# Kernel optimization log

Hardware: AMD Instinct MI355X
Metric: run time of the kernel (lower is better)

Reference implementation:

```python
import jax, jax.numpy as jnp
import numpy as np

EPS = 1e-6
NUM_HEADS = 16


def _layer_norm(x, alpha, beta):
    # Custom LN: unbiased std, divides by (std + eps) -- matches source exactly.
    mean = jnp.mean(x, axis=-1, keepdims=True)
    std = jnp.std(x, axis=-1, keepdims=True, ddof=1)
    return alpha * (x - mean) / (std + EPS) + beta


def _mha(x, wq, bq, wk, bk, wv, bv, wo, bo):
    B, S, D = x.shape
    H = NUM_HEADS
    Dh = D // H
    q = (x @ wq.T + bq).reshape(B, S, H, Dh)
    k = (x @ wk.T + bk).reshape(B, S, H, Dh)
    v = (x @ wv.T + bv).reshape(B, S, H, Dh)
    scores = jnp.einsum('bqhd,bkhd->bhqk', q, k) / jnp.sqrt(jnp.float32(Dh)).astype(x.dtype)
    p = jax.nn.softmax(scores, axis=-1)
    out = jnp.einsum('bhqk,bkhd->bqhd', p, v).reshape(B, S, D)
    return out @ wo.T + bo


def _ffn(x, w1, b1, w2, b2):
    return jax.nn.relu(x @ w1.T + b1) @ w2.T + b2


def setup_inputs() -> dict:
    key = jax.random.key(0)
    ks = jax.random.split(key, 8)
    B, S, D, Hf = 8, 1024, 1024, 4096
    s = lambda d: 1.0 / np.sqrt(d)
    return {
        'x': jax.random.normal(ks[0], (B, S, D), jnp.float32),
        'src_mask': jnp.ones((B, 1, 1, S), jnp.int32),
        'wq': jax.random.normal(ks[1], (D, D), jnp.float32) * s(D),
        'bq': jnp.zeros((D,), jnp.float32),
        'wk': jax.random.normal(ks[2], (D, D), jnp.float32) * s(D),
        'bk': jnp.zeros((D,), jnp.float32),
        'wv': jax.random.normal(ks[3], (D, D), jnp.float32) * s(D),
        'bv': jnp.zeros((D,), jnp.float32),
        'wo': jax.random.normal(ks[4], (D, D), jnp.float32) * s(D),
        'bo': jnp.zeros((D,), jnp.float32),
        'w1': jax.random.normal(ks[5], (Hf, D), jnp.float32) * s(D),
        'b1': jnp.zeros((Hf,), jnp.float32),
        'w2': jax.random.normal(ks[6], (D, Hf), jnp.float32) * s(Hf),
        'b2': jnp.zeros((D,), jnp.float32),
        'alpha': jnp.ones((D,), jnp.float32),
        'beta': jnp.zeros((D,), jnp.float32),
    }


def reference(x, src_mask, wq, bq, wk, bk, wv, bv, wo, bo, w1, b1, w2, b2, alpha, beta):
    # src_mask is unused in the source's attention implementation (faithful).
    # Pre-LN residual block 1: attention (shared LN params alpha/beta).
    x = x + _mha(_layer_norm(x, alpha, beta), wq, bq, wk, bk, wv, bv, wo, bo)
    # Pre-LN residual block 2: feed-forward (same shared LN instance).
    x = x + _ffn(_layer_norm(x, alpha, beta), w1, b1, w2, b2)
    return x
```

## Files before the change

kernel.cpp:

```cpp
#include <hip/hip_runtime.h>
#include <hip/hip_bf16.h>
#include <stdint.h>

typedef __bf16 bf16;
typedef __attribute__((ext_vector_type(8))) __bf16 bf16x8;
typedef __attribute__((ext_vector_type(4))) __bf16 bf16x4;
typedef __attribute__((ext_vector_type(4))) float floatx4;

typedef __attribute__((address_space(3))) uint32_t* lds_u32p;
typedef const __attribute__((address_space(1))) uint32_t* glb_u32p;

__device__ __forceinline__ void gload16(void* lds, const void* g) {
  __builtin_amdgcn_global_load_lds((glb_u32p)(uintptr_t)g,
                                   (lds_u32p)(uintptr_t)lds, 16, 0, 0);
}

__global__ __launch_bounds__(256) void detect_kernel(
    const unsigned short* __restrict__ xr, int* __restrict__ flag) {
  __shared__ int cnt;
  if (threadIdx.x == 0) cnt = 0;
  __syncthreads();
  int c = 0;
  for (int i = threadIdx.x; i < 8192; i += 256) {
    unsigned short e = (xr[i] >> 7) & 0xFF;
    if (e >= 0x90) ++c;
  }
  atomicAdd(&cnt, c);
  __syncthreads();
  if (threadIdx.x == 0) *flag = (cnt > 64) ? 1 : 0;
}

#define NCONV 14
struct ConvArgs {
  const void* src[NCONV];
  bf16* dst[NCONV];
  int nelem[NCONV];
  int bstart[NCONV + 1];
};

__global__ __launch_bounds__(256) void convert_kernel(ConvArgs a, const int* __restrict__ flag) {
  const int isf = *flag;
  const int bx = blockIdx.x;
  int t = 0;
  #pragma unroll
  for (int i = 1; i < NCONV; ++i)
    if (bx >= a.bstart[i]) t = i;
  const int base = (bx - a.bstart[t]) * 2048 + threadIdx.x * 8;
  if (base >= a.nelem[t]) return;
  if (isf) {
    const float* s = (const float*)a.src[t] + base;
    const float4 x0 = *reinterpret_cast<const float4*>(s);
    const float4 x1 = *reinterpret_cast<const float4*>(s + 4);
    bf16x8 o;
    o[0] = (bf16)x0.x; o[1] = (bf16)x0.y; o[2] = (bf16)x0.z; o[3] = (bf16)x0.w;
    o[4] = (bf16)x1.x; o[5] = (bf16)x1.y; o[6] = (bf16)x1.z; o[7] = (bf16)x1.w;
    *reinterpret_cast<bf16x8*>(a.dst[t] + base) = o;
  } else {
    *reinterpret_cast<bf16x8*>(a.dst[t] + base) =
        *reinterpret_cast<const bf16x8*>((const bf16*)a.src[t] + base);
  }
}

__global__ __launch_bounds__(256) void ln_kernel(
    const void* __restrict__ x, const bf16* __restrict__ alpha,
    const bf16* __restrict__ beta, bf16* __restrict__ y,
    const int* __restrict__ flag, int x_ext) {
  const int isf = *flag;
  const int row = blockIdx.x;
  const int tid = threadIdx.x;

  float v0, v1, v2, v3;
  if (x_ext && isf) {
    const float4 xv = *reinterpret_cast<const float4*>(
        (const float*)x + (size_t)row * 1024 + tid * 4);
    v0 = xv.x; v1 = xv.y; v2 = xv.z; v3 = xv.w;
  } else {
    const bf16x4 xv = *reinterpret_cast<const bf16x4*>(
        (const bf16*)x + (size_t)row * 1024 + tid * 4);
    v0 = (float)xv[0]; v1 = (float)xv[1]; v2 = (float)xv[2]; v3 = (float)xv[3];
  }
  float s = v0 + v1 + v2 + v3;
  float ss = v0 * v0 + v1 * v1 + v2 * v2 + v3 * v3;
  #pragma unroll
  for (int off = 32; off > 0; off >>= 1) {
    s += __shfl_down(s, off);
    ss += __shfl_down(ss, off);
  }
  __shared__ float red[8];
  __shared__ float s_mean, s_inv;
  const int w = tid >> 6, lane = tid & 63;
  if (lane == 0) { red[w] = s; red[4 + w] = ss; }
  __syncthreads();
  if (tid == 0) {
    float S = red[0] + red[1] + red[2] + red[3];
    float SS = red[4] + red[5] + red[6] + red[7];
    float mean = S * (1.0f / 1024.0f);
    float var = (SS - 1024.0f * mean * mean) * (1.0f / 1023.0f);
    var = fmaxf(var, 0.0f);
    s_mean = mean;
    s_inv = 1.0f / (sqrtf(var) + 1e-6f);
  }
  __syncthreads();
  const float mean = s_mean, inv = s_inv;
  const bf16x4 av = *reinterpret_cast<const bf16x4*>(alpha + tid * 4);
  const bf16x4 bv = *reinterpret_cast<const bf16x4*>(beta + tid * 4);
  bf16x4 out;
  out[0] = (bf16)((float)av[0] * (v0 - mean) * inv + (float)bv[0]);
  out[1] = (bf16)((float)av[1] * (v1 - mean) * inv + (float)bv[1]);
  out[2] = (bf16)((float)av[2] * (v2 - mean) * inv + (float)bv[2]);
  out[3] = (bf16)((float)av[3] * (v3 - mean) * inv + (float)bv[3]);
  *reinterpret_cast<bf16x4*>(y + (size_t)row * 1024 + tid * 4) = out;
}

template <bool RELU, bool RES>
__global__ __launch_bounds__(256) void gemm_bt(
    const bf16* __restrict__ A, const bf16* __restrict__ W,
    const bf16* __restrict__ bias, const void* __restrict__ res,
    void* __restrict__ C, int M, int N, int K,
    const int* __restrict__ flag, int res_ext, int out_ext, int row0) {
  __shared__ bf16 As[128 * 64];
  __shared__ bf16 Bs[128 * 64];
  const int isf = *flag;
  const int tid = threadIdx.x;
  const int m0 = blockIdx.x * 128, n0 = blockIdx.y * 128;
  const int wave = tid >> 6, lane = tid & 63;
  const int wm = (wave >> 1) * 64, wn = (wave & 1) * 64;
  const int lrow = lane & 15, quad = lane >> 4;

  const int srow = lane >> 3;
  const int gchunk = (lane & 7) ^ srow;
  const bf16* Ab = A + (size_t)m0 * K;
  const bf16* Wb = W + (size_t)n0 * K;

  floatx4 acc[4][4] = {};

  for (int k0 = 0; k0 < K; k0 += 64) {
    __syncthreads();
    #pragma unroll
    for (int t = 0; t < 4; ++t) {
      const int r = t * 32 + wave * 8;
      gload16(&As[r * 64], Ab + (size_t)(r + srow) * K + k0 + gchunk * 8);
      gload16(&Bs[r * 64], Wb + (size_t)(r + srow) * K + k0 + gchunk * 8);
    }
    __syncthreads();

    #pragma unroll
    for (int ks = 0; ks < 2; ++ks) {
      const int cswz = ((ks * 4 + quad) ^ (lrow & 7)) * 8;
      bf16x8 af[4], bw[4];
      #pragma unroll
      for (int i = 0; i < 4; ++i) {
        af[i] = *reinterpret_cast<const bf16x8*>(&As[(wm + i * 16 + lrow) * 64 + cswz]);
        bw[i] = *reinterpret_cast<const bf16x8*>(&Bs[(wn + i * 16 + lrow) * 64 + cswz]);
      }
      #pragma unroll
      for (int i = 0; i < 4; ++i)
        #pragma unroll
        for (int j = 0; j < 4; ++j)
          acc[i][j] = __builtin_amdgcn_mfma_f32_16x16x32_bf16(af[i], bw[j], acc[i][j], 0, 0, 0);
    }
  }

  #pragma unroll
  for (int j = 0; j < 4; ++j) {
    const int col = n0 + wn + j * 16 + lrow;
    const float bv = (float)bias[col];
    #pragma unroll
    for (int i = 0; i < 4; ++i) {
      #pragma unroll
      for (int r = 0; r < 4; ++r) {
        const int row = m0 + wm + i * 16 + quad * 4 + r;
        float v = acc[i][j][r] + bv;
        if (RELU) v = fmaxf(v, 0.0f);
        if (RES) {
          const size_t ridx = (size_t)row * N + col;
          v += (res_ext && isf) ? ((const float*)res)[ridx]
                                : (float)((const bf16*)res)[ridx];
        }
        const size_t oidx = (size_t)(row0 + row) * N + col;
        if (out_ext && isf) ((float*)C)[oidx] = v;
        else ((bf16*)C)[oidx] = (bf16)v;
      }
    }
  }
}

template <bool RELU, bool RES>
__global__ __launch_bounds__(256) void gemm_n64(
    const bf16* __restrict__ A, const bf16* __restrict__ W,
    const bf16* __restrict__ bias, const void* __restrict__ res,
    void* __restrict__ C, int M, int N, int K,
    const int* __restrict__ flag, int res_ext, int out_ext, int row0) {
  __shared__ bf16 As[128 * 64];
  __shared__ bf16 Bs[64 * 64];
  const int isf = *flag;
  const int tid = threadIdx.x;
  const int m0 = blockIdx.x * 128, n0 = blockIdx.y * 64;
  const int wave = tid >> 6, lane = tid & 63;
  const int wm = (wave >> 1) * 64, wn = (wave & 1) * 32;
  const int lrow = lane & 15, quad = lane >> 4;

  const int srow = lane >> 3;
  const int gchunk = (lane & 7) ^ srow;
  const bf16* Ab = A + (size_t)m0 * K;
  const bf16* Wb = W + (size_t)n0 * K;

  floatx4 acc[4][2] = {};

  for (int k0 = 0; k0 < K; k0 += 64) {
    __syncthreads();
    #pragma unroll
    for (int t = 0; t < 4; ++t) {
      const int r = t * 32 + wave * 8;
      gload16(&As[r * 64], Ab + (size_t)(r + srow) * K + k0 + gchunk * 8);
    }
    #pragma unroll
    for (int t = 0; t < 2; ++t) {
      const int r = t * 32 + wave * 8;
      gload16(&Bs[r * 64], Wb + (size_t)(r + srow) * K + k0 + gchunk * 8);
    }
    __syncthreads();

    #pragma unroll
    for (int ks = 0; ks < 2; ++ks) {
      const int cswz = ((ks * 4 + quad) ^ (lrow & 7)) * 8;
      bf16x8 af[4], bw[2];
      #pragma unroll
      for (int i = 0; i < 4; ++i)
        af[i] = *reinterpret_cast<const bf16x8*>(&As[(wm + i * 16 + lrow) * 64 + cswz]);
      #pragma unroll
      for (int j = 0; j < 2; ++j)
        bw[j] = *reinterpret_cast<const bf16x8*>(&Bs[(wn + j * 16 + lrow) * 64 + cswz]);
      #pragma unroll
      for (int i = 0; i < 4; ++i)
        #pragma unroll
        for (int j = 0; j < 2; ++j)
          acc[i][j] = __builtin_amdgcn_mfma_f32_16x16x32_bf16(af[i], bw[j], acc[i][j], 0, 0, 0);
    }
  }

  #pragma unroll
  for (int j = 0; j < 2; ++j) {
    const int col = n0 + wn + j * 16 + lrow;
    const float bv = (float)bias[col];
    #pragma unroll
    for (int i = 0; i < 4; ++i) {
      #pragma unroll
      for (int r = 0; r < 4; ++r) {
        const int row = m0 + wm + i * 16 + quad * 4 + r;
        float v = acc[i][j][r] + bv;
        if (RELU) v = fmaxf(v, 0.0f);
        if (RES) {
          const size_t ridx = (size_t)row * N + col;
          v += (res_ext && isf) ? ((const float*)res)[ridx]
                                : (float)((const bf16*)res)[ridx];
        }
        const size_t oidx = (size_t)(row0 + row) * N + col;
        if (out_ext && isf) ((float*)C)[oidx] = v;
        else ((bf16*)C)[oidx] = (bf16)v;
      }
    }
  }
}

__global__ __launch_bounds__(256) void gemm_qkv(
    const bf16* __restrict__ A,
    const bf16* __restrict__ Wq, const bf16* __restrict__ Wk, const bf16* __restrict__ Wv,
    const bf16* __restrict__ Bq, const bf16* __restrict__ Bk, const bf16* __restrict__ Bv,
    bf16* __restrict__ Oq, bf16* __restrict__ Ok, bf16* __restrict__ Ov) {
  const int z = blockIdx.z;
  const bf16* W = (z == 0) ? Wq : (z == 1) ? Wk : Wv;
  const bf16* bias = (z == 0) ? Bq : (z == 1) ? Bk : Bv;
  bf16* C = (z == 0) ? Oq : (z == 1) ? Ok : Ov;
  const int K = 1024, N = 1024;

  __shared__ bf16 As[128 * 64];
  __shared__ bf16 Bs[128 * 64];
  const int tid = threadIdx.x;
  const int m0 = blockIdx.x * 128, n0 = blockIdx.y * 128;
  const int wave = tid >> 6, lane = tid & 63;
  const int wm = (wave >> 1) * 64, wn = (wave & 1) * 64;
  const int lrow = lane & 15, quad = lane >> 4;

  const int srow = lane >> 3;
  const int gchunk = (lane & 7) ^ srow;
  const bf16* Ab = A + (size_t)m0 * K;
  const bf16* Wb = W + (size_t)n0 * K;

  floatx4 acc[4][4] = {};

  for (int k0 = 0; k0 < K; k0 += 64) {
    __syncthreads();
    #pragma unroll
    for (int t = 0; t < 4; ++t) {
      const int r = t * 32 + wave * 8;
      gload16(&As[r * 64], Ab + (size_t)(r + srow) * K + k0 + gchunk * 8);
      gload16(&Bs[r * 64], Wb + (size_t)(r + srow) * K + k0 + gchunk * 8);
    }
    __syncthreads();

    #pragma unroll
    for (int ks = 0; ks < 2; ++ks) {
      const int cswz = ((ks * 4 + quad) ^ (lrow & 7)) * 8;
      bf16x8 af[4], bw[4];
      #pragma unroll
      for (int i = 0; i < 4; ++i) {
        af[i] = *reinterpret_cast<const bf16x8*>(&As[(wm + i * 16 + lrow) * 64 + cswz]);
        bw[i] = *reinterpret_cast<const bf16x8*>(&Bs[(wn + i * 16 + lrow) * 64 + cswz]);
      }
      #pragma unroll
      for (int i = 0; i < 4; ++i)
        #pragma unroll
        for (int j = 0; j < 4; ++j)
          acc[i][j] = __builtin_amdgcn_mfma_f32_16x16x32_bf16(af[i], bw[j], acc[i][j], 0, 0, 0);
    }
  }

  #pragma unroll
  for (int j = 0; j < 4; ++j) {
    const int col = n0 + wn + j * 16 + lrow;
    const float bv = (float)bias[col];
    #pragma unroll
    for (int i = 0; i < 4; ++i) {
      #pragma unroll
      for (int r = 0; r < 4; ++r) {
        const int row = m0 + wm + i * 16 + quad * 4 + r;
        C[(size_t)row * N + col] = (bf16)(acc[i][j][r] + bv);
      }
    }
  }
}

__global__ __launch_bounds__(256) void attn_kernel(
    const bf16* __restrict__ Qg, const bf16* __restrict__ Kg,
    const bf16* __restrict__ Vg, bf16* __restrict__ Og) {
  __shared__ bf16 Ks[64][72];
  __shared__ bf16 Vts[64][72];
  __shared__ bf16 Ps[4][32][72];

  const int tid = threadIdx.x, wave = tid >> 6, lane = tid & 63;
  const int lrow = lane & 15, quad = lane >> 4;
  const int bq = blockIdx.x, h = blockIdx.y, b = blockIdx.z;
  const int q0 = bq * 128 + wave * 32;

  bf16x8 qa[2][2];
  #pragma unroll
  for (int t = 0; t < 2; ++t) {
    const bf16* qbase = Qg + (size_t)(b * 1024 + q0 + t * 16 + lrow) * 1024 + h * 64;
    qa[t][0] = *reinterpret_cast<const bf16x8*>(qbase + quad * 8);
    qa[t][1] = *reinterpret_cast<const bf16x8*>(qbase + 32 + quad * 8);
  }

  const int skp = tid >> 2, sdd = (tid & 3) * 16;
  const int vkp = tid & 63, vdg = wave * 16;

  floatx4 o[2][4] = {};
  float lsum[2][4] = {};

  for (int kc = 0; kc < 1024; kc += 64) {
    __syncthreads();
    {
      const bf16* ksrc = Kg + (size_t)(b * 1024 + kc + skp) * 1024 + h * 64 + sdd;
      *reinterpret_cast<bf16x8*>(&Ks[skp][sdd]) = *reinterpret_cast<const bf16x8*>(ksrc);
      *reinterpret_cast<bf16x8*>(&Ks[skp][sdd + 8]) = *reinterpret_cast<const bf16x8*>(ksrc + 8);

      const bf16* vsrc = Vg + (size_t)(b * 1024 + kc + vkp) * 1024 + h * 64 + vdg;
      bf16x8 v0 = *reinterpret_cast<const bf16x8*>(vsrc);
      bf16x8 v1 = *reinterpret_cast<const bf16x8*>(vsrc + 8);
      #pragma unroll
      for (int j = 0; j < 8; ++j) {
        Vts[vdg + j][vkp] = v0[j];
        Vts[vdg + 8 + j][vkp] = v1[j];
      }
    }
    __syncthreads();

    #pragma unroll
    for (int t = 0; t < 2; ++t) {
      floatx4 s[4] = {};
      #pragma unroll
      for (int kt = 0; kt < 4; ++kt) {
        bf16x8 kb0 = *reinterpret_cast<const bf16x8*>(&Ks[kt * 16 + lrow][quad * 8]);
        bf16x8 kb1 = *reinterpret_cast<const bf16x8*>(&Ks[kt * 16 + lrow][32 + quad * 8]);
        s[kt] = __builtin_amdgcn_mfma_f32_16x16x32_bf16(qa[t][0], kb0, s[kt], 0, 0, 0);
        s[kt] = __builtin_amdgcn_mfma_f32_16x16x32_bf16(qa[t][1], kb1, s[kt], 0, 0, 0);
      }
      #pragma unroll
      for (int r = 0; r < 4; ++r) {
        const float p0 = __expf(s[0][r] * 0.125f);
        const float p1 = __expf(s[1][r] * 0.125f);
        const float p2 = __expf(s[2][r] * 0.125f);
        const float p3 = __expf(s[3][r] * 0.125f);
        lsum[t][r] += (p0 + p1) + (p2 + p3);
        const int qr = t * 16 + quad * 4 + r;
        Ps[wave][qr][lrow] = (bf16)p0;
        Ps[wave][qr][16 + lrow] = (bf16)p1;
        Ps[wave][qr][32 + lrow] = (bf16)p2;
        Ps[wave][qr][48 + lrow] = (bf16)p3;
      }
    }

    __builtin_amdgcn_wave_barrier();

    #pragma unroll
    for (int t = 0; t < 2; ++t) {
      const bf16x8 pf0 = *reinterpret_cast<const bf16x8*>(&Ps[wave][t * 16 + lrow][quad * 8]);
      const bf16x8 pf1 = *reinterpret_cast<const bf16x8*>(&Ps[wave][t * 16 + lrow][32 + quad * 8]);
      #pragma unroll
      for (int j = 0; j < 4; ++j) {
        bf16x8 vb0 = *reinterpret_cast<const bf16x8*>(&Vts[j * 16 + lrow][quad * 8]);
        bf16x8 vb1 = *reinterpret_cast<const bf16x8*>(&Vts[j * 16 + lrow][32 + quad * 8]);
        o[t][j] = __builtin_amdgcn_mfma_f32_16x16x32_bf16(pf0, vb0, o[t][j], 0, 0, 0);
        o[t][j] = __builtin_amdgcn_mfma_f32_16x16x32_bf16(pf1, vb1, o[t][j], 0, 0, 0);
      }
    }
  }

  #pragma unroll
  for (int t = 0; t < 2; ++t) {
    #pragma unroll
    for (int r = 0; r < 4; ++r) {
      float l = lsum[t][r];
      #pragma unroll
      for (int off = 1; off < 16; off <<= 1) l += __shfl_xor(l, off);
      const float inv = 1.0f / l;
      const size_t qrow = (size_t)(b * 1024 + q0 + t * 16 + quad * 4 + r);
      #pragma unroll
      for (int j = 0; j < 4; ++j)
        Og[qrow * 1024 + h * 64 + j * 16 + lrow] = (bf16)(o[t][j][r] * inv);
    }
  }
}

extern "C" void kernel_launch(void* const* d_in, const int* in_sizes, int n_in,
                              void* d_out, int out_size, void* d_ws, size_t ws_size,
                              hipStream_t stream) {
  const void* p[16];
  {
    int j = 0;
    for (int i = 0; i < 16; ++i) {
      if (i == 1) {
        if (j < n_in && in_sizes[j] == 8192) p[i] = d_in[j++];
        else p[i] = nullptr;
        continue;
      }
      p[i] = (j < n_in) ? d_in[j++] : nullptr;
    }
  }
  const void* x = p[0];

  char* ws = (char*)d_ws;
  int* flag = (int*)ws;
  char* wsc = ws + 256;

  const int wsz[NCONV] = {1048576, 1048576, 1048576, 1048576, 4194304, 4194304,
                          1024, 1024, 1024, 1024, 4096, 1024, 1024, 1024};
  const int wsrc[NCONV] = {2, 4, 6, 8, 10, 12, 3, 5, 7, 9, 11, 13, 14, 15};
  ConvArgs ca;
  bf16* cptr[NCONV];
  size_t off = 0;
  int bacc = 0;
  for (int i = 0; i < NCONV; ++i) {
    cptr[i] = (bf16*)(wsc + off);
    off += (size_t)wsz[i] * sizeof(bf16);
    ca.src[i] = p[wsrc[i]];
    ca.dst[i] = cptr[i];
    ca.nelem[i] = wsz[i];
    ca.bstart[i] = bacc;
    bacc += (wsz[i] + 2047) / 2048;
  }
  ca.bstart[NCONV] = bacc;
  const bf16 *wq_c = cptr[0], *wk_c = cptr[1], *wv_c = cptr[2], *wo_c = cptr[3];
  const bf16 *w1_c = cptr[4], *w2_c = cptr[5];
  const bf16 *bq_c = cptr[6], *bk_c = cptr[7], *bv_c = cptr[8], *bo_c = cptr[9];
  const bf16 *b1_c = cptr[10], *b2_c = cptr[11], *al_c = cptr[12], *be_c = cptr[13];

  char* base = wsc + ((off + 255) & ~(size_t)255);
  const size_t SZ = (size_t)8192 * 1024 * sizeof(bf16);
  bf16* s1 = (bf16*)(base);
  bf16* s0 = (bf16*)(base + SZ);
  bf16* s2 = (bf16*)(base + 2 * SZ);
  bf16* s3 = (bf16*)(base + 3 * SZ);
  bf16* Kb = (bf16*)d_out;

  const int M = 8192, D = 1024, HF = 4096;

  detect_kernel<<<1, 256, 0, stream>>>((const unsigned short*)x, flag);
  convert_kernel<<<bacc, 256, 0, stream>>>(ca, flag);
  ln_kernel<<<8192, 256, 0, stream>>>(x, al_c, be_c, s0, flag, 1);
  gemm_qkv<<<dim3(M / 128, D / 128, 3), 256, 0, stream>>>(
      s0, wq_c, wk_c, wv_c, bq_c, bk_c, bv_c, s1, Kb, s2);
  attn_kernel<<<dim3(8, 16, 8), 256, 0, stream>>>(s1, Kb, s2, s3);
  gemm_n64<false, true><<<dim3(M / 128, D / 64), 256, 0, stream>>>(
      s3, wo_c, bo_c, x, s1, M, D, D, flag, 1, 0, 0);
  ln_kernel<<<8192, 256, 0, stream>>>(s1, al_c, be_c, s0, flag, 0);

  const size_t used = (size_t)(base - ws) + 4 * SZ;
  if (ws_size >= used + (size_t)M * HF * sizeof(bf16)) {
    bf16* Hf = (bf16*)(base + 4 * SZ);
    gemm_bt<true, false><<<dim3(M / 128, HF / 128), 256, 0, stream>>>(
        s0, w1_c, b1_c, nullptr, Hf, M, HF, D, flag, 0, 0, 0);
    gemm_n64<false, true><<<dim3(M / 128, D / 64), 256, 0, stream>>>(
        Hf, w2_c, b2_c, s1, d_out, M, D, HF, flag, 0, 1, 0);
  } else {
    bf16* H = s2;
    for (int hh = 0; hh < 2; ++hh) {
      const size_t ro = (size_t)hh * 4096 * 1024;
      gemm_bt<true, false><<<dim3(32, 32), 256, 0, stream>>>(
          s0 + ro, w1_c, b1_c, nullptr, H, 4096, HF, D, flag, 0, 0, 0);
      gemm_n64<false, true><<<dim3(32, D / 64), 256, 0, stream>>>(
          H, w2_c, b2_c, s1 + ro, d_out, 4096, D, HF, flag, 0, 1, hh * 4096);
    }
  }
}
```

Measured before the change: 513.4 us.

## Add 256x256 double-buffered MFMA kernel for FFN first GEMM

Replaces the generic 128x128 GEMM used for the FFN up-projection with a dedicated 256x256-tile kernel using 512 threads, double-buffered LDS and interleaved async prefetch of the next K tile between MFMA groups. Larger tiles raise arithmetic intensity and cut global/LDS traffic per flop, and the staggered prefetch with priority raising overlaps loads with compute. It uses much more LDS per block, which limits occupancy, and hardcodes the problem dimensions.

```diff
diff --git a/kernel.cpp b/kernel.cpp
--- a/kernel.cpp
+++ b/kernel.cpp
@@ -263,6 +263,106 @@
   }
 }
 
+__global__ __launch_bounds__(512, 2) void gemm_ffn1_256(
+    const bf16* __restrict__ A, const bf16* __restrict__ W,
+    const bf16* __restrict__ bias, bf16* __restrict__ C) {
+  constexpr int K = 1024, N = 4096, NK = K / 64;
+  __shared__ bf16 As[2][256 * 64];
+  __shared__ bf16 Bs[2][256 * 64];
+  const int tid = threadIdx.x;
+  const int wave = tid >> 6, lane = tid & 63;
+  const int m0 = blockIdx.x * 256, n0 = blockIdx.y * 256;
+  const int wm = (wave >> 2) * 128;
+  const int wn = (wave & 3) * 64;
+  const int lrow = lane & 15, quad = lane >> 4;
+  const int srow = lane >> 3;
+  const int gchunk = (lane & 7) ^ srow;
+  const bf16* Ab = A + (size_t)m0 * K;
+  const bf16* Wb = W + (size_t)n0 * K;
+  const int awr = wave * 32;
+
+  floatx4 acc[8][4] = {};
+
+  auto piece = [&](int kt, int nb, int p) {
+    const bf16* G = (p < 2) ? Ab : Wb;
+    bf16* L = (p < 2) ? &As[nb][0] : &Bs[nb][0];
+    #pragma unroll
+    for (int t = (p & 1) * 2; t < (p & 1) * 2 + 2; ++t) {
+      const int r = awr + t * 8;
+      gload16(L + r * 64, G + (size_t)(r + srow) * K + kt * 64 + gchunk * 8);
+    }
+  };
+
+  piece(0, 0, 0); piece(0, 0, 1); piece(0, 0, 2); piece(0, 0, 3);
+
+  for (int kt = 0; kt < NK; ++kt) {
+    const int cur = kt & 1, nb = cur ^ 1;
+    const bool pre = (kt + 1 < NK);
+
+    __builtin_amdgcn_sched_barrier(0);
+    __builtin_amdgcn_s_barrier();
+    __builtin_amdgcn_sched_barrier(0);
+    if (pre) {
+      piece(kt + 1, nb, 0);
+      asm volatile("s_waitcnt vmcnt(2)" ::: "memory");
+    } else {
+      asm volatile("s_waitcnt vmcnt(0)" ::: "memory");
+    }
+    __builtin_amdgcn_sched_barrier(0);
+    __builtin_amdgcn_s_barrier();
+    __builtin_amdgcn_sched_barrier(0);
+
+    bf16x8 bw[4][2];
+    #pragma unroll
+    for (int j = 0; j < 4; ++j) {
+      const int row = wn + j * 16 + lrow;
+      #pragma unroll
+      for (int ks = 0; ks < 2; ++ks) {
+        const int c = (ks * 4 + quad) ^ (lrow & 7);
+        bw[j][ks] = *reinterpret_cast<const bf16x8*>(&Bs[cur][row * 64 + c * 8]);
+      }
+    }
+    #pragma unroll
+    for (int p = 0; p < 4; ++p) {
+      bf16x8 af[2][2];
+      #pragma unroll
+      for (int il = 0; il < 2; ++il) {
+        const int row = wm + (p * 2 + il) * 16 + lrow;
+        #pragma unroll
+        for (int ks = 0; ks < 2; ++ks) {
+          const int c = (ks * 4 + quad) ^ (lrow & 7);
+          af[il][ks] = *reinterpret_cast<const bf16x8*>(&As[cur][row * 64 + c * 8]);
+        }
+      }
+      if (pre && p < 3) piece(kt + 1, nb, p + 1);
+      __builtin_amdgcn_s_setprio(1);
+      #pragma unroll
+      for (int il = 0; il < 2; ++il)
+        #pragma unroll
+        for (int j = 0; j < 4; ++j)
+          #pragma unroll
+          for (int ks = 0; ks < 2; ++ks)
+            acc[p * 2 + il][j] = __builtin_amdgcn_mfma_f32_16x16x32_bf16(
+                af[il][ks], bw[j][ks], acc[p * 2 + il][j], 0, 0, 0);
+      __builtin_amdgcn_s_setprio(0);
+    }
+  }
+
+  #pragma unroll
+  for (int j = 0; j < 4; ++j) {
+    const int col = n0 + wn + j * 16 + lrow;
+    const float bv = (float)bias[col];
+    #pragma unroll
+    for (int i = 0; i < 8; ++i) {
+      #pragma unroll
+      for (int r = 0; r < 4; ++r) {
+        const int row = m0 + wm + i * 16 + quad * 4 + r;
+        C[(size_t)row * N + col] = (bf16)fmaxf(acc[i][j][r] + bv, 0.0f);
+      }
+    }
+  }
+}
+
 __global__ __launch_bounds__(256) void gemm_qkv(
     const bf16* __restrict__ A,
     const bf16* __restrict__ Wq, const bf16* __restrict__ Wk, const bf16* __restrict__ Wv,
@@ -498,8 +598,7 @@
   const size_t used = (size_t)(base - ws) + 4 * SZ;
   if (ws_size >= used + (size_t)M * HF * sizeof(bf16)) {
     bf16* Hf = (bf16*)(base + 4 * SZ);
-    gemm_bt<true, false><<<dim3(M / 128, HF / 128), 256, 0, stream>>>(
-        s0, w1_c, b1_c, nullptr, Hf, M, HF, D, flag, 0, 0, 0);
+    gemm_ffn1_256<<<dim3(M / 256, HF / 256), 512, 0, stream>>>(s0, w1_c, b1_c, Hf);
     gemm_n64<false, true><<<dim3(M / 128, D / 64), 256, 0, stream>>>(
         Hf, w2_c, b2_c, s1, d_out, M, D, HF, flag, 0, 1, 0);
   } else {
```

Result: faster. 495.6 us (-3.5%).
